# Performance work log

Measured on AMD Instinct MI355X. Metric: run time of the kernel, lower is better.

## Reference

```python
import jax, jax.numpy as jnp
import numpy as np

N_NODES = 50000


def setup_inputs() -> dict:
    key = jax.random.key(0)
    k1, k2, k3, k4 = jax.random.split(key, 4)
    x = jax.random.normal(k1, (N_NODES, 256), dtype=jnp.float32)
    edge_index = jax.random.randint(k2, (2, 800000), 0, N_NODES, dtype=jnp.int64)
    W1 = jax.random.normal(k3, (256, 128), dtype=jnp.float32) * (1.0 / np.sqrt(256))
    b1 = jnp.zeros((128,), dtype=jnp.float32)
    W2 = jax.random.normal(k4, (128, 16), dtype=jnp.float32) * (1.0 / np.sqrt(128))
    b2 = jnp.zeros((16,), dtype=jnp.float32)
    return {"x": x, "edge_index": edge_index, "W1": W1, "b1": b1, "W2": W2, "b2": b2}


def _gcn_norm(edge_index, num_nodes):
    # add self-loops, then symmetric normalization D^-1/2 A D^-1/2 (PyG GCNConv default)
    loop = jnp.arange(num_nodes, dtype=edge_index.dtype)
    src = jnp.concatenate([edge_index[0], loop])
    dst = jnp.concatenate([edge_index[1], loop])
    deg = jax.ops.segment_sum(jnp.ones_like(dst, dtype=jnp.float32), dst, num_segments=num_nodes)
    dinv = jnp.where(deg > 0, jax.lax.rsqrt(deg), 0.0)
    norm = dinv[src] * dinv[dst]  # [E+N]
    return src, dst, norm


def _gcn_conv(h, W, b, src, dst, norm, num_nodes):
    h = h @ W                             # linear before propagate
    msg = h[src] * norm[:, None]          # gather + edge scaling
    agg = jax.ops.segment_sum(msg, dst, num_segments=num_nodes)  # scatter-add
    return agg + b


def reference(x, edge_index, W1, b1, W2, b2):
    n = x.shape[0]
    src, dst, norm = _gcn_norm(edge_index, n)
    h = jax.nn.relu(_gcn_conv(x, W1, b1, src, dst, norm, n))
    # F.dropout(training=False) is identity in eval mode
    out = _gcn_conv(h, W2, b2, src, dst, norm, n)
    return jax.nn.log_softmax(out, axis=1)
```

## Files before the change

### kernel.cpp

```cpp
#include <hip/hip_runtime.h>
#include <hip/hip_bf16.h>
#include <math.h>


#define FIN 256
#define FH  128
#define FO  16
#define SCAN_CHUNK 1024

typedef unsigned int uint;
typedef unsigned short ushort;
typedef __attribute__((ext_vector_type(8))) short bf16x8;
typedef __attribute__((ext_vector_type(4))) float f32x4;

static __device__ __forceinline__ ushort f2bf(float f) {
    __hip_bfloat16 b = __float2bfloat16(f);
    return *reinterpret_cast<ushort*>(&b);
}
static __device__ __forceinline__ float bf2f(ushort u) {
    return __uint_as_float(((uint)u) << 16);
}

__global__ __launch_bounds__(256) void GCN_zerowprep_k(int* __restrict__ count, int N,
                                                       const float* __restrict__ W1,
                                                       ushort* __restrict__ whT,
                                                       ushort* __restrict__ wlT,
                                                       int nZero) {
    if ((int)blockIdx.x < nZero) {
        int i = blockIdx.x * 256 + threadIdx.x;
        if (i < N) count[i] = 0;
    } else {
        int i = (blockIdx.x - nZero) * 256 + threadIdx.x;
        int k = i >> 7, c = i & 127;
        float w = W1[i];
        ushort hh = f2bf(w);
        ushort hl = f2bf(w - bf2f(hh));
        whT[c * 256 + k] = hh;
        wlT[c * 256 + k] = hl;
    }
}

#define G1_BR 64
#define G1_KC 32

__global__ __launch_bounds__(256, 4) void GCN_histgemm_k(
        const float* __restrict__ x, const ushort* __restrict__ whT,
        const ushort* __restrict__ wlT, ushort* __restrict__ h1,
        const int* __restrict__ edge, int* __restrict__ count,
        int* __restrict__ rank, int N, int E, int nGemm) {
    __shared__ __align__(16) ushort xh_s[G1_BR * G1_KC];
    __shared__ __align__(16) ushort xl_s[G1_BR * G1_KC];
    __shared__ __align__(16) ushort wh_s[FH * G1_KC];
    __shared__ __align__(16) ushort wl_s[FH * G1_KC];
    int tid = threadIdx.x;

    if ((int)blockIdx.x >= nGemm) {
        int i = (blockIdx.x - nGemm) * 256 + tid;
        if (i < E) rank[i] = atomicAdd(&count[edge[E + i]], 1);
        return;
    }

    int row0 = blockIdx.x * G1_BR;
    int ln = tid & 63;
    int w  = tid >> 6;
    int ln15 = ln & 15;
    int q16  = ln >> 4;

    f32x4 acc[4][2];
    #pragma unroll
    for (int mr = 0; mr < 4; mr++)
        #pragma unroll
        for (int nc = 0; nc < 2; nc++) acc[mr][nc] = (f32x4){0.f, 0.f, 0.f, 0.f};

    for (int kc = 0; kc < FIN; kc += G1_KC) {
        #pragma unroll
        for (int j = 0; j < 2; j++) {
            int u = tid + j * 256;
            int r = u >> 3, kq = u & 7;
            int gr = row0 + r;
            float4 v = make_float4(0.f, 0.f, 0.f, 0.f);
            if (gr < N) v = *(const float4*)&x[(size_t)gr * FIN + kc + kq * 4];
            ushort h0 = f2bf(v.x), h1v = f2bf(v.y), h2 = f2bf(v.z), h3 = f2bf(v.w);
            ushort l0 = f2bf(v.x - bf2f(h0));
            ushort l1 = f2bf(v.y - bf2f(h1v));
            ushort l2 = f2bf(v.z - bf2f(h2));
            ushort l3 = f2bf(v.w - bf2f(h3));
            uint2 hw, lw;
            hw.x = (uint)h0 | ((uint)h1v << 16);
            hw.y = (uint)h2 | ((uint)h3 << 16);
            lw.x = (uint)l0 | ((uint)l1 << 16);
            lw.y = (uint)l2 | ((uint)l3 << 16);
            int byte = (r * 64 + kq * 8) ^ (((r >> 1) & 3) << 4);
            *(uint2*)((char*)xh_s + byte) = hw;
            *(uint2*)((char*)xl_s + byte) = lw;
        }
        #pragma unroll
        for (int j = 0; j < 2; j++) {
            int u = tid + j * 256;
            int c = u >> 2, ku = u & 3;
            uint4 vh = *(const uint4*)&whT[(size_t)c * 256 + kc + ku * 8];
            uint4 vl = *(const uint4*)&wlT[(size_t)c * 256 + kc + ku * 8];
            int byte = (c * 64 + ku * 16) ^ (((c >> 1) & 3) << 4);
            *(uint4*)((char*)wh_s + byte) = vh;
            *(uint4*)((char*)wl_s + byte) = vl;
        }
        __syncthreads();

        bf16x8 ah[4], al[4], bh[2], bl[2];
        #pragma unroll
        for (int mr = 0; mr < 4; mr++) {
            int r = mr * 16 + ln15;
            int byte = r * 64 + ((q16 * 16) ^ (((r >> 1) & 3) << 4));
            ah[mr] = *(const bf16x8*)((const char*)xh_s + byte);
            al[mr] = *(const bf16x8*)((const char*)xl_s + byte);
        }
        #pragma unroll
        for (int nc = 0; nc < 2; nc++) {
            int c = w * 32 + nc * 16 + ln15;
            int byte = c * 64 + ((q16 * 16) ^ (((c >> 1) & 3) << 4));
            bh[nc] = *(const bf16x8*)((const char*)wh_s + byte);
            bl[nc] = *(const bf16x8*)((const char*)wl_s + byte);
        }
        #pragma unroll
        for (int mr = 0; mr < 4; mr++)
            #pragma unroll
            for (int nc = 0; nc < 2; nc++) {
                acc[mr][nc] = __builtin_amdgcn_mfma_f32_16x16x32_bf16(
                    ah[mr], bh[nc], acc[mr][nc], 0, 0, 0);
                acc[mr][nc] = __builtin_amdgcn_mfma_f32_16x16x32_bf16(
                    al[mr], bh[nc], acc[mr][nc], 0, 0, 0);
                acc[mr][nc] = __builtin_amdgcn_mfma_f32_16x16x32_bf16(
                    ah[mr], bl[nc], acc[mr][nc], 0, 0, 0);
            }
        __syncthreads();
    }

    #pragma unroll
    for (int mr = 0; mr < 4; mr++) {
        #pragma unroll
        for (int nc = 0; nc < 2; nc++) {
            int cw = w * 32 + nc * 16 + ln15;
            #pragma unroll
            for (int j = 0; j < 4; j++) {
                int gr = row0 + mr * 16 + q16 * 4 + j;
                if (gr < N) h1[(size_t)gr * FH + cw] = f2bf(acc[mr][nc][j]);
            }
        }
    }
}

__global__ __launch_bounds__(256) void GCN_bsum_k(const int* __restrict__ count,
                                                  int* __restrict__ bsum, int N) {
    int tid = threadIdx.x;
    int i0 = blockIdx.x * SCAN_CHUNK + tid * 4;
    int s = 0;
    if (i0 + 3 < N) {
        int4 c = *(const int4*)&count[i0];
        s = c.x + c.y + c.z + c.w + 4;
    } else {
        for (int j = 0; j < 4; j++)
            if (i0 + j < N) s += count[i0 + j] + 1;
    }
    __shared__ int red[256];
    red[tid] = s;
    __syncthreads();
    for (int st = 128; st > 0; st >>= 1) {
        if (tid < st) red[tid] += red[tid + st];
        __syncthreads();
    }
    if (tid == 0) bsum[blockIdx.x] = red[0];
}

__global__ __launch_bounds__(256) void GCN_scan2_k(const int* __restrict__ count,
                                                   const int* __restrict__ bsum,
                                                   int2* __restrict__ rd2,
                                                   int2* __restrict__ edata, int N) {
    int tid = threadIdx.x;
    int b = blockIdx.x;
    int i0 = b * SCAN_CHUNK + tid * 4;

    int v0 = 0, v1 = 0, v2 = 0, v3 = 0;
    if (i0 + 3 < N) {
        int4 c = *(const int4*)&count[i0];
        v0 = c.x + 1; v1 = c.y + 1; v2 = c.z + 1; v3 = c.w + 1;
    } else {
        if (i0 + 0 < N) v0 = count[i0 + 0] + 1;
        if (i0 + 1 < N) v1 = count[i0 + 1] + 1;
        if (i0 + 2 < N) v2 = count[i0 + 2] + 1;
        if (i0 + 3 < N) v3 = count[i0 + 3] + 1;
    }
    int lsum = v0 + v1 + v2 + v3;

    __shared__ int red[256];
    int offp = 0;
    for (int t = tid; t < b; t += 256) offp += bsum[t];
    red[tid] = offp;
    __syncthreads();
    for (int st = 128; st > 0; st >>= 1) {
        if (tid < st) red[tid] += red[tid + st];
        __syncthreads();
    }
    int blockOff = red[0];
    __syncthreads();

    __shared__ int ssum[256];
    ssum[tid] = lsum;
    __syncthreads();
    for (int off = 1; off < 256; off <<= 1) {
        int t = (tid >= off) ? ssum[tid - off] : 0;
        __syncthreads();
        ssum[tid] += t;
        __syncthreads();
    }
    int r = blockOff + (tid == 0 ? 0 : ssum[tid - 1]);

    #pragma unroll
    for (int q = 0; q < 4; q++) {
        int v = i0 + q;
        if (v < N) {
            int c = (q == 0) ? v0 : (q == 1) ? v1 : (q == 2) ? v2 : v3;
            float dv = rsqrtf((float)c);
            rd2[v] = make_int2(r, __float_as_int(dv));
            edata[r] = make_int2(v, __float_as_int(dv * dv));
            r += c;
        }
    }
    if (b == gridDim.x - 1 && tid == 255) rd2[N] = make_int2(blockOff + ssum[255], 0);
}

__global__ __launch_bounds__(256) void GCN_fill_k(const int* __restrict__ edge,
                                                  const int* __restrict__ rank,
                                                  const int2* __restrict__ rd2,
                                                  int2* __restrict__ edata, int E) {
    int i = blockIdx.x * 256 + threadIdx.x;
    if (i >= E) return;
    int s = edge[i];
    int d = edge[E + i];
    int rk = rank[i];
    int2 rdd = rd2[d];
    float ds = __int_as_float(rd2[s].y);
    edata[rdd.x + 1 + rk] = make_int2(s, __float_as_int(ds * __int_as_float(rdd.y)));
}

__global__ __launch_bounds__(256) void GCN_agg1gemm2_k(
        const ushort* __restrict__ h1, const int2* __restrict__ rd2,
        const int2* __restrict__ ed, const float* __restrict__ b1,
        const float* __restrict__ W2, ushort* __restrict__ h2b, int N) {
    __shared__ float w2s[FH][FO];
    __shared__ float hs[16][FH + 4];
    int tid = threadIdx.x;
    #pragma unroll
    for (int j = 0; j < (FH * FO) / 256; j++) {
        int i = tid + j * 256;
        w2s[i >> 4][i & 15] = W2[i];
    }

    int node0 = blockIdx.x * 16;
    int local = tid >> 4;
    int j = tid & 15;
    int node = node0 + local;

    if (node < N) {
        int beg = rd2[node].x, end = rd2[node + 1].x;
        const uint4* hp = (const uint4*)h1;

        float a[8];
        #pragma unroll
        for (int t = 0; t < 8; t++) a[t] = 0.f;

        int i = beg;
        for (; i + 4 <= end; i += 4) {
            int2 e0 = ed[i + 0], e1 = ed[i + 1], e2 = ed[i + 2], e3 = ed[i + 3];
            float w0 = __int_as_float(e0.y), w1 = __int_as_float(e1.y);
            float w2 = __int_as_float(e2.y), w3 = __int_as_float(e3.y);
            uint4 g0 = hp[(size_t)e0.x * 16 + j];
            uint4 g1 = hp[(size_t)e1.x * 16 + j];
            uint4 g2 = hp[(size_t)e2.x * 16 + j];
            uint4 g3 = hp[(size_t)e3.x * 16 + j];
            #pragma unroll
            for (int q = 0; q < 4; q++) {
                uint u0 = (&g0.x)[q], u1 = (&g1.x)[q], u2 = (&g2.x)[q], u3 = (&g3.x)[q];
                a[q*2+0] += __uint_as_float(u0 << 16) * w0;
                a[q*2+1] += __uint_as_float(u0 & 0xFFFF0000u) * w0;
                a[q*2+0] += __uint_as_float(u1 << 16) * w1;
                a[q*2+1] += __uint_as_float(u1 & 0xFFFF0000u) * w1;
                a[q*2+0] += __uint_as_float(u2 << 16) * w2;
                a[q*2+1] += __uint_as_float(u2 & 0xFFFF0000u) * w2;
                a[q*2+0] += __uint_as_float(u3 << 16) * w3;
                a[q*2+1] += __uint_as_float(u3 & 0xFFFF0000u) * w3;
            }
        }
        for (; i < end; i++) {
            int2 e = ed[i];
            float w = __int_as_float(e.y);
            uint4 g = hp[(size_t)e.x * 16 + j];
            #pragma unroll
            for (int q = 0; q < 4; q++) {
                uint u = (&g.x)[q];
                a[q*2+0] += __uint_as_float(u << 16) * w;
                a[q*2+1] += __uint_as_float(u & 0xFFFF0000u) * w;
            }
        }

        const float4* bp = (const float4*)b1;
        float4 bb0 = bp[j * 2 + 0];
        float4 bb1 = bp[j * 2 + 1];
        float4 o0, o1;
        o0.x = fmaxf(a[0] + bb0.x, 0.f);
        o0.y = fmaxf(a[1] + bb0.y, 0.f);
        o0.z = fmaxf(a[2] + bb0.z, 0.f);
        o0.w = fmaxf(a[3] + bb0.w, 0.f);
        o1.x = fmaxf(a[4] + bb1.x, 0.f);
        o1.y = fmaxf(a[5] + bb1.y, 0.f);
        o1.z = fmaxf(a[6] + bb1.z, 0.f);
        o1.w = fmaxf(a[7] + bb1.w, 0.f);
        *(float4*)&hs[local][j * 8 + 0] = o0;
        *(float4*)&hs[local][j * 8 + 4] = o1;
    }
    __syncthreads();

    float acc = 0.f;
    #pragma unroll 8
    for (int k = 0; k < FH; k++) acc += hs[local][k] * w2s[k][j];
    if (node < N) h2b[(size_t)node * FO + j] = f2bf(acc);
}

__global__ __launch_bounds__(256) void GCN_agg2_k(const ushort* __restrict__ h2b,
                                                  const int2* __restrict__ rd2,
                                                  const int2* __restrict__ ed,
                                                  const float* __restrict__ b2,
                                                  float* __restrict__ out, int N) {
    int tid = threadIdx.x;
    int node = blockIdx.x * 32 + (tid >> 3);
    if (node >= N) return;
    int f2 = tid & 7;
    int beg = rd2[node].x, end = rd2[node + 1].x;
    const uint* hp = (const uint*)h2b;
    float a0 = 0.f, a1 = 0.f;
    int i = beg;
    for (; i + 4 <= end; i += 4) {
        int2 e0 = ed[i + 0], e1 = ed[i + 1], e2 = ed[i + 2], e3 = ed[i + 3];
        uint u0 = hp[(size_t)e0.x * 8 + f2];
        uint u1 = hp[(size_t)e1.x * 8 + f2];
        uint u2 = hp[(size_t)e2.x * 8 + f2];
        uint u3 = hp[(size_t)e3.x * 8 + f2];
        float w0 = __int_as_float(e0.y), w1 = __int_as_float(e1.y);
        float w2 = __int_as_float(e2.y), w3 = __int_as_float(e3.y);
        a0 += __uint_as_float(u0 << 16) * w0 + __uint_as_float(u1 << 16) * w1
            + __uint_as_float(u2 << 16) * w2 + __uint_as_float(u3 << 16) * w3;
        a1 += __uint_as_float(u0 & 0xFFFF0000u) * w0 + __uint_as_float(u1 & 0xFFFF0000u) * w1
            + __uint_as_float(u2 & 0xFFFF0000u) * w2 + __uint_as_float(u3 & 0xFFFF0000u) * w3;
    }
    for (; i < end; i++) {
        int2 e = ed[i];
        uint u = hp[(size_t)e.x * 8 + f2];
        float w = __int_as_float(e.y);
        a0 += __uint_as_float(u << 16) * w;
        a1 += __uint_as_float(u & 0xFFFF0000u) * w;
    }
    float2 bb = ((const float2*)b2)[f2];
    float v0 = a0 + bb.x;
    float v1 = a1 + bb.y;
    float mx = fmaxf(v0, v1);
    #pragma unroll
    for (int m = 4; m >= 1; m >>= 1) mx = fmaxf(mx, __shfl_xor(mx, m, 8));
    float s = expf(v0 - mx) + expf(v1 - mx);
    #pragma unroll
    for (int m = 4; m >= 1; m >>= 1) s += __shfl_xor(s, m, 8);
    float ls = logf(s);
    float2 o = make_float2(v0 - mx - ls, v1 - mx - ls);
    ((float2*)out)[(size_t)node * 8 + f2] = o;
}

extern "C" void kernel_launch(void* const* d_in, const int* in_sizes, int n_in,
                              void* d_out, int out_size, void* d_ws, size_t ws_size,
                              hipStream_t stream) {
    (void)n_in; (void)out_size; (void)ws_size;
    const float* x  = (const float*)d_in[0];
    const int*   edp = (const int*)d_in[1];
    const float* W1 = (const float*)d_in[2];
    const float* b1 = (const float*)d_in[3];
    const float* W2 = (const float*)d_in[4];
    const float* b2 = (const float*)d_in[5];
    float* out = (float*)d_out;

    int N = in_sizes[0] / FIN;
    int E = in_sizes[1] / 2;
    int M = E + N;
    int nScanBlocks = (N + SCAN_CHUNK - 1) / SCAN_CHUNK;

    char* p = (char*)d_ws;
    auto take = [&](size_t bytes) -> char* {
        char* r = p;
        p += (bytes + 255) & ~(size_t)255;
        return r;
    };
    int*    count  = (int*)take((size_t)N * 4);
    int*    rank   = (int*)take((size_t)E * 4);
    int2*   rd2    = (int2*)take((size_t)(N + 1) * 8);
    int*    bsum   = (int*)take((size_t)nScanBlocks * 4);
    int2*   edata  = (int2*)take((size_t)M * 8);
    ushort* whT    = (ushort*)take((size_t)FH * FIN * 2);
    ushort* wlT    = (ushort*)take((size_t)FH * FIN * 2);
    ushort* h1     = (ushort*)take((size_t)N * FH * 2);
    ushort* h2b    = (ushort*)take((size_t)N * FO * 2);

    int eBlocks = (E + 255) / 256;
    int nGemm   = (N + G1_BR - 1) / G1_BR;
    int nZero   = (N + 255) / 256;

    GCN_zerowprep_k<<<nZero + (FIN * FH) / 256, 256, 0, stream>>>(
        count, N, W1, whT, wlT, nZero);
    GCN_histgemm_k<<<nGemm + eBlocks, 256, 0, stream>>>(
        x, whT, wlT, h1, edp, count, rank, N, E, nGemm);
    GCN_bsum_k<<<nScanBlocks, 256, 0, stream>>>(count, bsum, N);
    GCN_scan2_k<<<nScanBlocks, 256, 0, stream>>>(count, bsum, rd2, edata, N);
    GCN_fill_k<<<eBlocks, 256, 0, stream>>>(edp, rank, rd2, edata, E);
    GCN_agg1gemm2_k<<<(N + 15) / 16, 256, 0, stream>>>(h1, rd2, edata, b1, W2, h2b, N);
    GCN_agg2_k<<<(N + 31) / 32, 256, 0, stream>>>(h2b, rd2, edata, b2, out, N);
}
```

Measured before the change: 121.5 us.

## Replace global atomic degree histogram with chunked shared-memory histograms

The per-edge global atomicAdd that built degree counts and edge ranks is replaced. Edges are split into 32 chunks and destination nodes into ranges that fit in shared memory, and each block builds an LDS histogram for one chunk/range pair. A new kernel prefix-sums the per-chunk histograms to get per-node counts and chunk offsets. The fill kernel then redoes the LDS atomics to get local ranks. This removes contended global atomics and the rank array, but each block rescans its whole edge chunk for every node range and adds a 6.4 MB chunk-histogram array.

```diff
diff --git a/kernel.cpp b/kernel.cpp
--- a/kernel.cpp
+++ b/kernel.cpp
@@ -7,6 +7,8 @@
 #define FH  128
 #define FO  16
 #define SCAN_CHUNK 1024
+#define NCHUNK 32
+#define QPR_MAX 6272
 
 typedef unsigned int uint;
 typedef unsigned short ushort;
@@ -21,45 +23,55 @@
     return __uint_as_float(((uint)u) << 16);
 }
 
-__global__ __launch_bounds__(256) void GCN_zerowprep_k(int* __restrict__ count, int N,
-                                                       const float* __restrict__ W1,
-                                                       ushort* __restrict__ whT,
-                                                       ushort* __restrict__ wlT,
-                                                       int nZero) {
-    if ((int)blockIdx.x < nZero) {
-        int i = blockIdx.x * 256 + threadIdx.x;
-        if (i < N) count[i] = 0;
-    } else {
-        int i = (blockIdx.x - nZero) * 256 + threadIdx.x;
-        int k = i >> 7, c = i & 127;
-        float w = W1[i];
-        ushort hh = f2bf(w);
-        ushort hl = f2bf(w - bf2f(hh));
-        whT[c * 256 + k] = hh;
-        wlT[c * 256 + k] = hl;
-    }
+__global__ __launch_bounds__(256) void GCN_wprep_k(const float* __restrict__ W1,
+                                                   ushort* __restrict__ whT,
+                                                   ushort* __restrict__ wlT) {
+    int i = blockIdx.x * 256 + threadIdx.x;
+    int k = i >> 7, c = i & 127;
+    float w = W1[i];
+    ushort hh = f2bf(w);
+    ushort hl = f2bf(w - bf2f(hh));
+    whT[c * 256 + k] = hh;
+    wlT[c * 256 + k] = hl;
 }
 
 #define G1_BR 64
 #define G1_KC 32
 
-__global__ __launch_bounds__(256, 4) void GCN_histgemm_k(
+__global__ __launch_bounds__(256, 4) void GCN_gemmhrank_k(
         const float* __restrict__ x, const ushort* __restrict__ whT,
         const ushort* __restrict__ wlT, ushort* __restrict__ h1,
-        const int* __restrict__ edge, int* __restrict__ count,
-        int* __restrict__ rank, int N, int E, int nGemm) {
-    __shared__ __align__(16) ushort xh_s[G1_BR * G1_KC];
-    __shared__ __align__(16) ushort xl_s[G1_BR * G1_KC];
-    __shared__ __align__(16) ushort wh_s[FH * G1_KC];
-    __shared__ __align__(16) ushort wl_s[FH * G1_KC];
+        const int* __restrict__ edge, int* __restrict__ chunkhist,
+        int N, int E, int nGemm, int nRange, int qpr, int ech) {
+    __shared__ __align__(16) char smem[QPR_MAX * 4];
     int tid = threadIdx.x;
 
     if ((int)blockIdx.x >= nGemm) {
-        int i = (blockIdx.x - nGemm) * 256 + tid;
-        if (i < E) rank[i] = atomicAdd(&count[edge[E + i]], 1);
+        int bid = blockIdx.x - nGemm;
+        int c = bid / nRange, r = bid % nRange;
+        int* lhist = (int*)smem;
+        for (int j = tid; j < qpr; j += 256) lhist[j] = 0;
+        __syncthreads();
+        int base = c * ech;
+        int lim = base + ech; if (lim > E) lim = E;
+        int r0 = r * qpr;
+        for (int i = base + tid; i < lim; i += 256) {
+            int d = edge[E + i];
+            int dd = d - r0;
+            if ((unsigned)dd < (unsigned)qpr) atomicAdd(&lhist[dd], 1);
+        }
+        __syncthreads();
+        for (int j = tid; j < qpr; j += 256) {
+            int d = r0 + j;
+            if (d < N) chunkhist[(size_t)c * N + d] = lhist[j];
+        }
         return;
     }
 
+    ushort* xh_s = (ushort*)smem;
+    ushort* xl_s = (ushort*)(smem + 4096);
+    ushort* wh_s = (ushort*)(smem + 8192);
+    ushort* wl_s = (ushort*)(smem + 16384);
     int row0 = blockIdx.x * G1_BR;
     int ln = tid & 63;
     int w  = tid >> 6;
@@ -149,20 +161,39 @@
     }
 }
 
-__global__ __launch_bounds__(256) void GCN_bsum_k(const int* __restrict__ count,
-                                                  int* __restrict__ bsum, int N) {
-    int tid = threadIdx.x;
-    int i0 = blockIdx.x * SCAN_CHUNK + tid * 4;
-    int s = 0;
-    if (i0 + 3 < N) {
-        int4 c = *(const int4*)&count[i0];
-        s = c.x + c.y + c.z + c.w + 4;
+__global__ __launch_bounds__(256) void GCN_chpfxbsum_k(int* __restrict__ chunkhist,
+                                                       int* __restrict__ count,
+                                                       int* __restrict__ bsum,
+                                                       int N) {
+    int tid = threadIdx.x;
+    int d0 = blockIdx.x * SCAN_CHUNK + tid * 4;
+    int local = 0;
+    if (d0 + 3 < N) {
+        int4 run = make_int4(0, 0, 0, 0);
+        for (int c = 0; c < NCHUNK; c++) {
+            int4* p = (int4*)&chunkhist[(size_t)c * N + d0];
+            int4 v = *p;
+            *p = run;
+            run.x += v.x; run.y += v.y; run.z += v.z; run.w += v.w;
+        }
+        *(int4*)&count[d0] = run;
+        local = run.x + run.y + run.z + run.w + 4;
     } else {
-        for (int j = 0; j < 4; j++)
-            if (i0 + j < N) s += count[i0 + j] + 1;
+        for (int q = 0; q < 4; q++) {
+            int d = d0 + q;
+            if (d < N) {
+                int run = 0;
+                for (int c = 0; c < NCHUNK; c++) {
+                    int* p = &chunkhist[(size_t)c * N + d];
+                    int v = *p; *p = run; run += v;
+                }
+                count[d] = run;
+                local += run + 1;
+            }
+        }
     }
     __shared__ int red[256];
-    red[tid] = s;
+    red[tid] = local;
     __syncthreads();
     for (int st = 128; st > 0; st >>= 1) {
         if (tid < st) red[tid] += red[tid + st];
@@ -229,17 +260,31 @@
 }
 
 __global__ __launch_bounds__(256) void GCN_fill_k(const int* __restrict__ edge,
-                                                  const int* __restrict__ rank,
+                                                  const int* __restrict__ chunkhist,
                                                   const int2* __restrict__ rd2,
-                                                  int2* __restrict__ edata, int E) {
-    int i = blockIdx.x * 256 + threadIdx.x;
-    if (i >= E) return;
-    int s = edge[i];
-    int d = edge[E + i];
-    int rk = rank[i];
-    int2 rdd = rd2[d];
-    float ds = __int_as_float(rd2[s].y);
-    edata[rdd.x + 1 + rk] = make_int2(s, __float_as_int(ds * __int_as_float(rdd.y)));
+                                                  int2* __restrict__ edata,
+                                                  int N, int E, int nRange,
+                                                  int qpr, int ech) {
+    __shared__ int lhist[QPR_MAX];
+    int tid = threadIdx.x;
+    int c = blockIdx.x / nRange, r = blockIdx.x % nRange;
+    for (int j = tid; j < qpr; j += 256) lhist[j] = 0;
+    __syncthreads();
+    int base = c * ech;
+    int lim = base + ech; if (lim > E) lim = E;
+    int r0 = r * qpr;
+    for (int i = base + tid; i < lim; i += 256) {
+        int d = edge[E + i];
+        int dd = d - r0;
+        if ((unsigned)dd < (unsigned)qpr) {
+            int lrank = atomicAdd(&lhist[dd], 1);
+            int s = edge[i];
+            int2 rdd = rd2[d];
+            float ds = __int_as_float(rd2[s].y);
+            int slot = rdd.x + 1 + chunkhist[(size_t)c * N + d] + lrank;
+            edata[slot] = make_int2(s, __float_as_int(ds * __int_as_float(rdd.y)));
+        }
+    }
 }
 
 __global__ __launch_bounds__(256) void GCN_agg1gemm2_k(
@@ -388,6 +433,9 @@
     int E = in_sizes[1] / 2;
     int M = E + N;
     int nScanBlocks = (N + SCAN_CHUNK - 1) / SCAN_CHUNK;
+    int nRange = (N + QPR_MAX - 1) / QPR_MAX;
+    int qpr = (N + nRange - 1) / nRange;
+    int ech = (E + NCHUNK - 1) / NCHUNK;
 
     char* p = (char*)d_ws;
     auto take = [&](size_t bytes) -> char* {
@@ -395,27 +443,25 @@
         p += (bytes + 255) & ~(size_t)255;
         return r;
     };
-    int*    count  = (int*)take((size_t)N * 4);
-    int*    rank   = (int*)take((size_t)E * 4);
-    int2*   rd2    = (int2*)take((size_t)(N + 1) * 8);
-    int*    bsum   = (int*)take((size_t)nScanBlocks * 4);
-    int2*   edata  = (int2*)take((size_t)M * 8);
-    ushort* whT    = (ushort*)take((size_t)FH * FIN * 2);
-    ushort* wlT    = (ushort*)take((size_t)FH * FIN * 2);
-    ushort* h1     = (ushort*)take((size_t)N * FH * 2);
-    ushort* h2b    = (ushort*)take((size_t)N * FO * 2);
-
-    int eBlocks = (E + 255) / 256;
-    int nGemm   = (N + G1_BR - 1) / G1_BR;
-    int nZero   = (N + 255) / 256;
-
-    GCN_zerowprep_k<<<nZero + (FIN * FH) / 256, 256, 0, stream>>>(
-        count, N, W1, whT, wlT, nZero);
-    GCN_histgemm_k<<<nGemm + eBlocks, 256, 0, stream>>>(
-        x, whT, wlT, h1, edp, count, rank, N, E, nGemm);
-    GCN_bsum_k<<<nScanBlocks, 256, 0, stream>>>(count, bsum, N);
+    int*    count     = (int*)take((size_t)N * 4);
+    int*    chunkhist = (int*)take((size_t)NCHUNK * N * 4);
+    int2*   rd2       = (int2*)take((size_t)(N + 1) * 8);
+    int*    bsum      = (int*)take((size_t)nScanBlocks * 4);
+    int2*   edata     = (int2*)take((size_t)M * 8);
+    ushort* whT       = (ushort*)take((size_t)FH * FIN * 2);
+    ushort* wlT       = (ushort*)take((size_t)FH * FIN * 2);
+    ushort* h1        = (ushort*)take((size_t)N * FH * 2);
+    ushort* h2b       = (ushort*)take((size_t)N * FO * 2);
+
+    int nGemm  = (N + G1_BR - 1) / G1_BR;
+    int nHrank = NCHUNK * nRange;
+
+    GCN_wprep_k<<<(FIN * FH) / 256, 256, 0, stream>>>(W1, whT, wlT);
+    GCN_gemmhrank_k<<<nGemm + nHrank, 256, 0, stream>>>(
+        x, whT, wlT, h1, edp, chunkhist, N, E, nGemm, nRange, qpr, ech);
+    GCN_chpfxbsum_k<<<nScanBlocks, 256, 0, stream>>>(chunkhist, count, bsum, N);
     GCN_scan2_k<<<nScanBlocks, 256, 0, stream>>>(count, bsum, rd2, edata, N);
-    GCN_fill_k<<<eBlocks, 256, 0, stream>>>(edp, rank, rd2, edata, E);
+    GCN_fill_k<<<nHrank, 256, 0, stream>>>(edp, chunkhist, rd2, edata, N, E, nRange, qpr, ech);
     GCN_agg1gemm2_k<<<(N + 15) / 16, 256, 0, stream>>>(h1, rd2, edata, b1, W2, h2b, N);
     GCN_agg2_k<<<(N + 31) / 32, 256, 0, stream>>>(h2b, rd2, edata, b2, out, N);
 }
```

Result: slower. 178.5 us (+46.8%).
